# Kernel tuning notes

Hardware: AMD Instinct MI355X
Metric: run time of the kernel (lower is better)

Reference implementation:

```python
import jax, jax.numpy as jnp
import numpy as np

N, E, IN, OUT, R, B = 20000, 640000, 128, 128, 64, 16


def setup_inputs() -> dict:
    key = jax.random.key(0)
    ks = jax.random.split(key, 9)
    xav_w = float(np.sqrt(2.0 / (IN + OUT)))  # xavier-uniform-ish scale
    xav_c = float(np.sqrt(2.0 / (R + B)))
    return {
        "x": jax.random.normal(ks[0], (N, IN), jnp.float32),
        "weight": jax.random.normal(ks[1], (B, IN, OUT), jnp.float32) * xav_w,
        "w_comp": jax.random.normal(ks[2], (R, B), jnp.float32) * xav_c,
        "h_bias": jnp.zeros((OUT,), jnp.float32),
        "loop_weight": jax.random.normal(ks[3], (IN, OUT), jnp.float32) * xav_w,
        "norm": jax.random.uniform(ks[4], (E, 1), jnp.float32),
        "src": jax.random.randint(ks[5], (E,), 0, N, jnp.int32),
        "dst": jax.random.randint(ks[6], (E,), 0, N, jnp.int32),
        "etypes": jax.random.randint(ks[7], (E,), 0, R, jnp.int32),
    }


def reference(x, weight, w_comp, h_bias, loop_weight, norm, src, dst, etypes):
    # Basis composition: per-relation weights W_rel[r] = sum_b w_comp[r,b] * weight[b]
    W_rel = jnp.einsum("rb,bio->rio", w_comp, weight)          # [R, IN, OUT]
    # Project every node through every relation weight (N*R << per-edge bmm
    # of E gathered [IN,OUT] matrices; same math as bmm_maybe_select).
    h_all = jnp.einsum("ni,rio->nro", x, W_rel)                 # [N, R, OUT]
    # Per-edge message: msg_e = x[src_e] @ W_rel[etype_e], scaled by norm
    msg = h_all[src, etypes] * norm                              # [E, OUT]
    # fn.sum aggregation to destination nodes
    agg = jax.ops.segment_sum(msg, dst, num_segments=x.shape[0])  # [N, OUT]
    out = agg + h_bias + x @ loop_weight                          # bias + self-loop
    return jax.nn.relu(out)                                       # activation; dropout p=0
```

## Files before the change

### kernel.cpp

```cpp
#include <hip/hip_runtime.h>

#define N_NODES 20000
#define E_EDGES 640000
#define R_REL   64
#define B_BASES 16
#define NSEG    128
#define SEGLEN  (E_EDGES / NSEG)
#define RH      10000
#define NBPR    16
#define QG      ((2 * NSEG) / 16)

typedef __attribute__((ext_vector_type(4))) float f32x4;
typedef __attribute__((ext_vector_type(8))) _Float16 half8;

__device__ inline float h2f(unsigned short v) {
    _Float16 h; __builtin_memcpy(&h, &v, 2); return (float)h;
}
__device__ inline unsigned short f2h(float f) {
    _Float16 h = (_Float16)f; unsigned short v; __builtin_memcpy(&v, &h, 2); return v;
}

__device__ inline void gld_lds16(const void* g, void* l) {
    __builtin_amdgcn_global_load_lds(
        (const __attribute__((address_space(1))) void*)g,
        (__attribute__((address_space(3))) void*)l, 16, 0, 0);
}


__global__ void k_wrelh(const float* weight, const float* w_comp, unsigned short* wt_h)
{
    __shared__ float tile[32][33];
    __shared__ float wcS[B_BASES];
    int r  = blockIdx.x >> 4;
    int ti = (blockIdx.x >> 2) & 3;
    int tj = blockIdx.x & 3;
    int tx = threadIdx.x & 31, ty = threadIdx.x >> 5;
    if (threadIdx.x < B_BASES) wcS[threadIdx.x] = w_comp[r * B_BASES + threadIdx.x];
    __syncthreads();
    float acc[4] = {0.f, 0.f, 0.f, 0.f};
    const float* wp = weight + (ti * 32) * 128 + tj * 32;
    for (int b = 0; b < B_BASES; b++) {
        float c = wcS[b];
        #pragma unroll
        for (int s = 0; s < 4; s++)
            acc[s] += c * wp[b * 16384 + (ty + s * 8) * 128 + tx];
    }
    #pragma unroll
    for (int s = 0; s < 4; s++) tile[ty + s * 8][tx] = acc[s];
    __syncthreads();
    unsigned short* dstp = wt_h + r * 16384 + (tj * 32) * 128 + ti * 32;
    #pragma unroll
    for (int s = 0; s < 4; s++)
        dstp[(ty + s * 8) * 128 + tx] = f2h(tile[tx][ty + s * 8]);
}

__global__ void k_lwh(const float* lw, unsigned short* lwT)
{
    __shared__ float tile[32][33];
    int ti = blockIdx.x >> 2, tj = blockIdx.x & 3;
    int tx = threadIdx.x & 31, ty = threadIdx.x >> 5;
    const float* srcp = lw + (ti * 32) * 128 + tj * 32;
    #pragma unroll
    for (int s = 0; s < 4; s++)
        tile[ty + s * 8][tx] = srcp[(ty + s * 8) * 128 + tx];
    __syncthreads();
    unsigned short* d = lwT + (tj * 32) * 128 + ti * 32;
    #pragma unroll
    for (int s = 0; s < 4; s++)
        d[(ty + s * 8) * 128 + tx] = f2h(tile[tx][ty + s * 8]);
}

__global__ void k_xhalf(const float* x, unsigned short* xh)
{
    int i4 = blockIdx.x * 256 + threadIdx.x;
    float4 v = ((const float4*)x)[i4];
    ushort4 o;
    o.x = f2h(v.x); o.y = f2h(v.y); o.z = f2h(v.z); o.w = f2h(v.w);
    ((ushort4*)xh)[i4] = o;
}

__global__ void k_histp(const int* etypes, const int* dst, int* hp, int* he)
{
    __shared__ int lh[RH];
    __shared__ int heL[R_REL];
    int t = threadIdx.x, q = blockIdx.x;
    int s = q >> 1, h = q & 1;
    for (int i = t; i < RH; i += 256) lh[i] = 0;
    if (t < R_REL) heL[t] = 0;
    __syncthreads();
    int e0 = s * SEGLEN;
    for (int k = t; k < SEGLEN; k += 256) {
        int e = e0 + k;
        int d = dst[e];
        unsigned ld = (unsigned)(d - h * RH);
        if (ld < RH) {
            atomicAdd(&lh[ld], 1);
            atomicAdd(&heL[etypes[e]], 1);
        }
    }
    __syncthreads();
    for (int i = t; i < RH; i += 256) hp[s * N_NODES + h * RH + i] = lh[i];
    if (t < R_REL) he[q * 64 + t] = heL[t];
}

__global__ void k_sumc(const int* hp, int* counts2)
{
    int n = blockIdx.x * 256 + threadIdx.x;
    if (n >= N_NODES) return;
    int s = 0;
    for (int q = 0; q < NSEG; q += 8) {
        int v[8];
        #pragma unroll
        for (int k = 0; k < 8; k++) v[k] = hp[(q + k) * N_NODES + n];
        #pragma unroll
        for (int k = 0; k < 8; k++) s += v[k];
    }
    counts2[n] = s;
}

__global__ void k_scan_all2(const int* he, const int* counts2,
                            int* offsets, int* off2, int* be)
{
    __shared__ int part[1024];
    __shared__ int psum[16][R_REL];
    __shared__ int offL[R_REL];
    int tid = threadIdx.x;
    int t = tid & 63;
    int g = tid >> 6;
    int vals[QG];
    int ps = 0;
    #pragma unroll
    for (int k = 0; k < QG; k++) {
        vals[k] = he[(g * QG + k) * 64 + t];
        ps += vals[k];
    }
    psum[g][t] = ps;
    __syncthreads();
    if (tid < 64) {
        int c = 0;
        #pragma unroll
        for (int gg = 0; gg < 16; gg++) c += psum[gg][t];
        int s1 = c;
        for (int d = 1; d < 64; d <<= 1) {
            int a1 = __shfl_up(s1, d);
            if (t >= d) s1 += a1;
        }
        offsets[t] = s1 - c;
        offL[t] = s1 - c;
        if (t == 63) offsets[64] = s1;
    }
    __syncthreads();
    {
        int run = offL[t];
        for (int gg = 0; gg < g; gg++) run += psum[gg][t];
        #pragma unroll
        for (int k = 0; k < QG; k++) {
            be[(g * QG + k) * 64 + t] = run;
            run += vals[k];
        }
    }
    int lo_i = tid * 20, hi_i = lo_i + 20;
    if (hi_i > N_NODES) hi_i = N_NODES;
    if (lo_i > N_NODES) lo_i = N_NODES;
    int s = 0;
    for (int i = lo_i; i < hi_i; i++) s += counts2[i];
    part[tid] = s;
    __syncthreads();
    for (int d = 1; d < 1024; d <<= 1) {
        int v = (tid >= d) ? part[tid - d] : 0;
        __syncthreads();
        part[tid] += v;
        __syncthreads();
    }
    int run = part[tid] - s;
    for (int i = lo_i; i < hi_i; i++) {
        off2[i] = run;
        run += counts2[i];
    }
    if (tid == 1023) off2[N_NODES] = run;
}

__global__ void k_segbase(const int* off2, int* hp)
{
    int n = blockIdx.x * 256 + threadIdx.x;
    if (n >= N_NODES) return;
    int run = off2[n];
    for (int q = 0; q < NSEG; q += 8) {
        int v[8];
        #pragma unroll
        for (int k = 0; k < 8; k++) v[k] = hp[(q + k) * N_NODES + n];
        #pragma unroll
        for (int k = 0; k < 8; k++) { hp[(q + k) * N_NODES + n] = run; run += v[k]; }
    }
}

__global__ void k_scatter3(const int* etypes, const int* dst, const int* src, const float* norm,
                           const int* hp, const int* be,
                           int* perm_src, float* pnorm, int* pos2)
{
    __shared__ int lbase[RH];
    __shared__ int ebase[R_REL];
    int t = threadIdx.x, q = blockIdx.x;
    int s = q >> 1, h = q & 1;
    for (int i = t; i < RH; i += 256) lbase[i] = hp[s * N_NODES + h * RH + i];
    if (t < R_REL) ebase[t] = be[q * 64 + t];
    __syncthreads();
    int e0 = s * SEGLEN;
    for (int k = t; k < SEGLEN; k += 256) {
        int e = e0 + k;
        int d = dst[e];
        unsigned ld = (unsigned)(d - h * RH);
        if (ld < RH) {
            int slot = atomicAdd(&lbase[ld], 1);
            int p = atomicAdd(&ebase[etypes[e]], 1);
            perm_src[p] = src[e];
            pnorm[p] = norm[e];
            pos2[p] = slot;
        }
    }
}

__global__ __launch_bounds__(256) void k_edge_mfma(
    const unsigned short* __restrict__ xh, const unsigned short* __restrict__ wt_h,
    const int* __restrict__ perm_src, const float* __restrict__ pnorm,
    const int* __restrict__ pos2, const int* __restrict__ offsets,
    unsigned short* __restrict__ msg)
{
    __shared__ __align__(16) char smemW[32768];
    int t = threadIdx.x, b = blockIdx.x;
    int r = b >> 4;
    int j = b & (NBPR - 1);
    int p0 = offsets[r], p1 = offsets[r + 1];
    int nch = (p1 - p0 + 63) >> 6;

    {
        const size_t rbase = (size_t)r * 16384;
        #pragma unroll
        for (int it = 0; it < 8; it++) {
            int s = it * 256 + t;
            int o = s >> 4, ch = s & 15;
            int jx = ch ^ (o & 15);
            gld_lds16(wt_h + rbase + o * 128 + jx * 8, smemW + s * 16);
        }
    }

    int l = t & 63, w = t >> 6;
    int lg = l >> 4, lr = l & 15;
    int wr = w >> 1, wc = w & 1;
    int rowA0 = wr * 32 + lr, rowA1 = rowA0 + 16;
    const half8* smW = (const half8*)smemW;

    int i = j;
    int sA0 = 0, sA1 = 0;
    if (i < nch) {
        int e0 = p0 + i * 64;
        int cnt = p1 - e0; if (cnt > 64) cnt = 64;
        sA0 = (rowA0 < cnt) ? perm_src[e0 + rowA0] : 0;
        sA1 = (rowA1 < cnt) ? perm_src[e0 + rowA1] : 0;
    }

    __syncthreads();

    while (i < nch) {
        int e0 = p0 + i * 64;
        int cnt = p1 - e0; if (cnt > 64) cnt = 64;

        int slotC[2][4]; float nrmC[2][4];
        #pragma unroll
        for (int a = 0; a < 2; a++)
            #pragma unroll
            for (int jj = 0; jj < 4; jj++) {
                int row = wr * 32 + a * 16 + lg * 4 + jj;
                bool vld = row < cnt;
                slotC[a][jj] = vld ? pos2[e0 + row] : -1;
                nrmC[a][jj]  = vld ? pnorm[e0 + row] : 0.0f;
            }

        const half8* xr0 = (const half8*)(xh + (size_t)sA0 * 128);
        const half8* xr1 = (const half8*)(xh + (size_t)sA1 * 128);
        half8 av0[4], av1[4];
        #pragma unroll
        for (int kk = 0; kk < 4; kk++) {
            av0[kk] = xr0[kk * 4 + lg];
            av1[kk] = xr1[kk * 4 + lg];
        }

        int inext = i + NBPR;
        if (inext < nch) {
            int e0n = p0 + inext * 64;
            int cntn = p1 - e0n; if (cntn > 64) cntn = 64;
            sA0 = (rowA0 < cntn) ? perm_src[e0n + rowA0] : 0;
            sA1 = (rowA1 < cntn) ? perm_src[e0n + rowA1] : 0;
        }

        f32x4 acc[2][4];
        #pragma unroll
        for (int a = 0; a < 2; a++)
            #pragma unroll
            for (int n = 0; n < 4; n++)
                acc[a][n] = {0.0f, 0.0f, 0.0f, 0.0f};

        #pragma unroll
        for (int kk = 0; kk < 4; kk++) {
            #pragma unroll
            for (int n = 0; n < 4; n++) {
                int o = wc * 64 + n * 16 + lr;
                half8 bv = smW[o * 16 + ((kk * 4 + lg) ^ (o & 15))];
                acc[0][n] = __builtin_amdgcn_mfma_f32_16x16x32_f16(av0[kk], bv, acc[0][n], 0, 0, 0);
                acc[1][n] = __builtin_amdgcn_mfma_f32_16x16x32_f16(av1[kk], bv, acc[1][n], 0, 0, 0);
            }
        }

        #pragma unroll
        for (int a = 0; a < 2; a++)
            #pragma unroll
            for (int jj = 0; jj < 4; jj++) {
                int slot = slotC[a][jj];
                if (slot >= 0) {
                    float nm = nrmC[a][jj];
                    unsigned int q0 = (unsigned int)f2h(acc[a][0][jj] * nm)
                                    | ((unsigned int)f2h(acc[a][1][jj] * nm) << 16);
                    unsigned int q1 = (unsigned int)f2h(acc[a][2][jj] * nm)
                                    | ((unsigned int)f2h(acc[a][3][jj] * nm) << 16);
                    uint2 ov; ov.x = q0; ov.y = q1;
                    *(uint2*)(msg + (size_t)slot * 128 + wc * 64 + lr * 4) = ov;
                }
            }
        i = inext;
    }
}

__global__ __launch_bounds__(256) void k_selfmfma(
    const unsigned short* __restrict__ xh, const unsigned short* __restrict__ lwT,
    float* __restrict__ out)
{
    __shared__ __align__(16) char smemW[32768];
    int t = threadIdx.x, b = blockIdx.x;
    int n0 = b * 64;

    #pragma unroll
    for (int it = 0; it < 8; it++) {
        int s = it * 256 + t;
        int o = s >> 4, ch = s & 15;
        int jx = ch ^ (o & 15);
        gld_lds16(lwT + o * 128 + jx * 8, smemW + s * 16);
    }

    int l = t & 63, w = t >> 6;
    int lg = l >> 4, lr = l & 15;
    int wr = w >> 1, wc = w & 1;
    int rowA0 = wr * 32 + lr, rowA1 = rowA0 + 16;
    int nA0 = n0 + rowA0; if (nA0 >= N_NODES) nA0 = N_NODES - 1;
    int nA1 = n0 + rowA1; if (nA1 >= N_NODES) nA1 = N_NODES - 1;
    const half8* xr0 = (const half8*)(xh + (size_t)nA0 * 128);
    const half8* xr1 = (const half8*)(xh + (size_t)nA1 * 128);
    half8 av0[4], av1[4];
    #pragma unroll
    for (int kk = 0; kk < 4; kk++) {
        av0[kk] = xr0[kk * 4 + lg];
        av1[kk] = xr1[kk * 4 + lg];
    }

    f32x4 acc[2][4];
    #pragma unroll
    for (int a = 0; a < 2; a++)
        #pragma unroll
        for (int n = 0; n < 4; n++)
            acc[a][n] = {0.0f, 0.0f, 0.0f, 0.0f};

    __syncthreads();

    const half8* smW = (const half8*)smemW;
    #pragma unroll
    for (int kk = 0; kk < 4; kk++) {
        #pragma unroll
        for (int n = 0; n < 4; n++) {
            int o = wc * 64 + n * 16 + lr;
            half8 bv = smW[o * 16 + ((kk * 4 + lg) ^ (o & 15))];
            acc[0][n] = __builtin_amdgcn_mfma_f32_16x16x32_f16(av0[kk], bv, acc[0][n], 0, 0, 0);
            acc[1][n] = __builtin_amdgcn_mfma_f32_16x16x32_f16(av1[kk], bv, acc[1][n], 0, 0, 0);
        }
    }

    #pragma unroll
    for (int a = 0; a < 2; a++)
        #pragma unroll
        for (int jj = 0; jj < 4; jj++) {
            int row = wr * 32 + a * 16 + lg * 4 + jj;
            int n = n0 + row;
            if (n < N_NODES) {
                float4 v;
                v.x = acc[a][0][jj]; v.y = acc[a][1][jj];
                v.z = acc[a][2][jj]; v.w = acc[a][3][jj];
                *(float4*)(out + (size_t)n * 128 + wc * 64 + lr * 4) = v;
            }
        }
}

__global__ void k_msgsum(const unsigned short* msg, const int* off2,
                         const float* bias, float* out)
{
    __shared__ float4 red[256];
    __shared__ float fin[128];
    int n = blockIdx.x, t = threadIdx.x;
    int m0 = off2[n], m1 = off2[n + 1];
    int rp = t >> 5, c = t & 31;
    float4 a; a.x = 0.f; a.y = 0.f; a.z = 0.f; a.w = 0.f;
    for (int j = m0 + rp; j < m1; j += 8) {
        uint2 v = *(const uint2*)(msg + (size_t)j * 128 + c * 4);
        a.x += h2f((unsigned short)(v.x & 0xffff));
        a.y += h2f((unsigned short)(v.x >> 16));
        a.z += h2f((unsigned short)(v.y & 0xffff));
        a.w += h2f((unsigned short)(v.y >> 16));
    }
    red[t] = a;
    __syncthreads();
    if (t < 128) {
        float4 b = red[t + 128];
        red[t].x += b.x; red[t].y += b.y; red[t].z += b.z; red[t].w += b.w;
    }
    __syncthreads();
    if (t < 64) {
        float4 b = red[t + 64];
        red[t].x += b.x; red[t].y += b.y; red[t].z += b.z; red[t].w += b.w;
    }
    __syncthreads();
    if (t < 32) {
        float4 v = red[t], b = red[t + 32];
        v.x += b.x; v.y += b.y; v.z += b.z; v.w += b.w;
        float4 o = *(const float4*)(out + (size_t)n * 128 + t * 4);
        v.x += o.x; v.y += o.y; v.z += o.z; v.w += o.w;
        int base = (t >> 4) * 64 + (t & 15);
        fin[base]      = v.x;
        fin[base + 16] = v.y;
        fin[base + 32] = v.z;
        fin[base + 48] = v.w;
    }
    __syncthreads();
    if (t < 32) {
        float4 f = ((const float4*)fin)[t];
        float4 bb = *(const float4*)(bias + t * 4);
        f.x += bb.x; f.y += bb.y; f.z += bb.z; f.w += bb.w;
        if (f.x < 0.f) f.x = 0.f;
        if (f.y < 0.f) f.y = 0.f;
        if (f.z < 0.f) f.z = 0.f;
        if (f.w < 0.f) f.w = 0.f;
        *(float4*)(out + (size_t)n * 128 + t * 4) = f;
    }
}


__global__ void k_wrel(const float* weight, const float* w_comp, float* W_rel)
{
    int idx = blockIdx.x * 256 + threadIdx.x;
    int r  = idx >> 14;
    int io = idx & 16383;
    float acc = 0.0f;
    for (int b = 0; b < B_BASES; b++)
        acc += w_comp[r * B_BASES + b] * weight[b * 16384 + io];
    W_rel[idx] = acc;
}

__global__ void k_zero(float* agg, int* counts, int* counts2)
{
    int idx = blockIdx.x * 256 + threadIdx.x;
    if (idx < N_NODES * 128) agg[idx] = 0.0f;
    if (idx < R_REL) counts[idx] = 0;
    if (idx < N_NODES) counts2[idx] = 0;
}

__global__ void k_hist(const int* etypes, int* counts)
{
    __shared__ int h[R_REL];
    int t = threadIdx.x;
    if (t < R_REL) h[t] = 0;
    __syncthreads();
    int e = blockIdx.x * 256 + t;
    atomicAdd(&h[etypes[e]], 1);
    __syncthreads();
    if (t < R_REL && h[t] != 0) atomicAdd(&counts[t], h[t]);
}

__global__ void k_scan(const int* counts, int* offsets, int* cursor, int* co)
{
    if (threadIdx.x == 0) {
        int run = 0, c = 0;
        for (int r = 0; r < R_REL; r++) {
            offsets[r] = run; cursor[r] = run; co[r] = c;
            run += counts[r];
            c   += (counts[r] + 63) >> 6;
        }
        offsets[R_REL] = run; co[R_REL] = c;
    }
}

__global__ void k_scatter(const int* etypes, int* cursor, int* perm)
{
    __shared__ int h[R_REL];
    __shared__ int base[R_REL];
    int t = threadIdx.x;
    if (t < R_REL) h[t] = 0;
    __syncthreads();
    int e = blockIdx.x * 256 + t;
    int et = etypes[e];
    int rank = atomicAdd(&h[et], 1);
    __syncthreads();
    if (t < R_REL && h[t] != 0) base[t] = atomicAdd(&cursor[t], h[t]);
    __syncthreads();
    perm[base[et] + rank] = e;
}

__global__ void k_edge_atomic(const float* x, const float* W_rel, const float* norm,
                              const int* src, const int* dst, const int* perm,
                              const int* offsets, const int* co, float* agg)
{
    __shared__ float4 WfS[2048];
    __shared__ float4 xsS[1024];
    __shared__ int coS[R_REL + 1];
    __shared__ int srcS[64], dstS[64];
    __shared__ float normS[64];
    int t = threadIdx.x, bid = blockIdx.x;
    if (t <= R_REL) coS[t] = co[t];
    __syncthreads();
    if (bid >= coS[R_REL]) return;
    int r = 0;
    while (bid >= coS[r + 1]) r++;
    int e0 = offsets[r] + (bid - coS[r]) * 64;
    int cnt = offsets[r + 1] - e0;
    if (cnt > 64) cnt = 64;
    if (t < 64) {
        if (t < cnt) {
            int eid = perm[e0 + t];
            srcS[t] = src[eid]; dstS[t] = dst[eid]; normS[t] = norm[eid];
        } else { srcS[t] = 0; dstS[t] = 0; normS[t] = 0.0f; }
    }
    const float* xsf = (const float*)xsS;
    int q  = t & 31;
    int eb = t >> 5;
    float4 acc[8];
    for (int k = 0; k < 8; k++) { acc[k].x = 0.f; acc[k].y = 0.f; acc[k].z = 0.f; acc[k].w = 0.f; }
    for (int h = 0; h < 2; h++) {
        __syncthreads();
        const float4* Wsrc = (const float4*)(W_rel + r * 16384 + h * 8192);
        for (int p = 0; p < 8; p++) WfS[p * 256 + t] = Wsrc[p * 256 + t];
        for (int p = 0; p < 4; p++) {
            int idx = p * 256 + t;
            int e = idx >> 4, c = idx & 15;
            xsS[idx] = ((const float4*)(x + srcS[e] * 128 + h * 64))[c];
        }
        __syncthreads();
        for (int i = 0; i < 64; i++) {
            float4 wv = WfS[i * 32 + q];
            for (int k = 0; k < 8; k++) {
                float xv = xsf[(eb + 8 * k) * 64 + i];
                acc[k].x += xv * wv.x;
                acc[k].y += xv * wv.y;
                acc[k].z += xv * wv.z;
                acc[k].w += xv * wv.w;
            }
        }
    }
    for (int k = 0; k < 8; k++) {
        int e = eb + 8 * k;
        if (e < cnt) {
            float nrm = normS[e];
            float* row = agg + dstS[e] * 128 + q * 4;
            atomicAdd(row + 0, acc[k].x * nrm);
            atomicAdd(row + 1, acc[k].y * nrm);
            atomicAdd(row + 2, acc[k].z * nrm);
            atomicAdd(row + 3, acc[k].w * nrm);
        }
    }
}

__global__ void k_out(const float* x, const float* loop_w, const float* agg,
                      const float* bias, float* out)
{
    __shared__ float xrow[128];
    int n = blockIdx.x;
    int o = threadIdx.x;
    xrow[o] = x[n * 128 + o];
    __syncthreads();
    float acc = 0.0f;
    for (int i = 0; i < 128; i++)
        acc += xrow[i] * loop_w[i * 128 + o];
    float val = acc + agg[n * 128 + o] + bias[o];
    if (val < 0.0f) val = 0.0f;
    out[n * 128 + o] = val;
}

extern "C" void kernel_launch(void* const* d_in, const int* in_sizes, int n_in,
                              void* d_out, int out_size, void* d_ws, size_t ws_size,
                              hipStream_t stream)
{
    const float* x      = (const float*)d_in[0];
    const float* weight = (const float*)d_in[1];
    const float* w_comp = (const float*)d_in[2];
    const float* h_bias = (const float*)d_in[3];
    const float* loop_w = (const float*)d_in[4];
    const float* norm   = (const float*)d_in[5];
    const int* src    = (const int*)d_in[6];
    const int* dst    = (const int*)d_in[7];
    const int* etypes = (const int*)d_in[8];
    float* out = (float*)d_out;

    char* ws = (char*)d_ws;
    size_t off = 0;
    float* W_rel = (float*)(ws + off); off += (size_t)R_REL * 16384 * 4;
    float* agg   = (float*)(ws + off); off += (size_t)N_NODES * 128 * 4;
    int* perm    = (int*)(ws + off);   off += (size_t)E_EDGES * 4;
    int* counts  = (int*)(ws + off);   off += 64 * 4;
    int* offsets = (int*)(ws + off);   off += 68 * 4;
    int* cursor  = (int*)(ws + off);   off += 64 * 4;
    int* co      = (int*)(ws + off);   off += 68 * 4;
    int* counts2 = (int*)(ws + off);   off += (size_t)N_NODES * 4;
    int* off2    = (int*)(ws + off);   off += (size_t)(N_NODES + 4) * 4;
    int* cursor2 = (int*)(ws + off);   off += (size_t)N_NODES * 4;
    int* pos2    = (int*)(ws + off);   off += (size_t)E_EDGES * 4;
    unsigned short* msg = (unsigned short*)(ws + off);
    size_t need_big = off + (size_t)E_EDGES * 128 * 2;
    int big = (ws_size >= need_big) ? 1 : 0;

    if (big) {
        unsigned short* wt_h = (unsigned short*)W_rel;
        char* wspare = (char*)W_rel + (size_t)2 * 1024 * 1024;
        unsigned short* lwT = (unsigned short*)wspare;
        unsigned short* xh = (unsigned short*)agg;
        float* pnorm = (float*)((char*)agg + (size_t)N_NODES * 128 * 2);
        int* perm_src = perm;
        int* hp = (int*)msg;
        int* he = (int*)((char*)msg + (size_t)NSEG * N_NODES * 4);
        int* be = (int*)((char*)he + (size_t)2 * NSEG * 64 * 4);

        k_wrelh<<<R_REL * 16, 256, 0, stream>>>(weight, w_comp, wt_h);
        k_lwh<<<16, 256, 0, stream>>>(loop_w, lwT);
        k_xhalf<<<(N_NODES * 128 / 4) / 256, 256, 0, stream>>>(x, xh);
        k_histp<<<2 * NSEG, 256, 0, stream>>>(etypes, dst, hp, he);
        k_sumc<<<(N_NODES + 255) / 256, 256, 0, stream>>>(hp, counts2);
        k_scan_all2<<<1, 1024, 0, stream>>>(he, counts2, offsets, off2, be);
        k_segbase<<<(N_NODES + 255) / 256, 256, 0, stream>>>(off2, hp);
        k_scatter3<<<2 * NSEG, 256, 0, stream>>>(etypes, dst, src, norm,
                                                 hp, be, perm_src, pnorm, pos2);
        k_edge_mfma<<<R_REL * NBPR, 256, 0, stream>>>(
            xh, wt_h, perm_src, pnorm, pos2, offsets, msg);
        k_selfmfma<<<(N_NODES + 63) / 64, 256, 0, stream>>>(xh, lwT, out);
        k_msgsum<<<N_NODES, 256, 0, stream>>>(msg, off2, h_bias, out);
    } else {
        k_wrel<<<(R_REL * 16384) / 256, 256, 0, stream>>>(weight, w_comp, W_rel);
        k_zero<<<(N_NODES * 128) / 256, 256, 0, stream>>>(agg, counts, counts2);
        k_hist<<<E_EDGES / 256, 256, 0, stream>>>(etypes, counts);
        k_scan<<<1, 64, 0, stream>>>(counts, offsets, cursor, co);
        k_scatter<<<E_EDGES / 256, 256, 0, stream>>>(etypes, cursor, perm);
        k_edge_atomic<<<E_EDGES / 64 + R_REL, 256, 0, stream>>>(
            x, W_rel, norm, src, dst, perm, offsets, co, agg);
        k_out<<<N_NODES, 128, 0, stream>>>(x, loop_w, agg, h_bias, out);
    }
}
```

Baseline: 274.8 us.

## Retile edge MFMA per-wave, prefetch gathered rows, double blocks per relation, fuse weight prep

The edge and self-loop MFMA kernels now give each wave 16 rows across all 128 output columns instead of a 2x2 wave split. Each lane writes 16-byte message stores, and the msgsum epilogue's column permutation is changed to match the new output layout. The edge kernel now prefetches the next chunk's gathered x rows into registers one iteration ahead, and blocks per relation go from 16 to 32 for more parallelism and latency hiding. The loop-weight transpose kernel is folded into the relation-weight kernel to save a launch. The trade-off is higher register pressure from the 8 accumulators plus the prefetch buffers, and each block reloading the 32KB weight tile into LDS twice as often.

Measured after the change: 266.4 us. 3.0% less time.

```diff
diff --git a/kernel.cpp b/kernel.cpp
--- a/kernel.cpp
+++ b/kernel.cpp
@@ -7,7 +7,7 @@
 #define NSEG    128
 #define SEGLEN  (E_EDGES / NSEG)
 #define RH      10000
-#define NBPR    16
+#define NBPR    32
 #define QG      ((2 * NSEG) / 16)
 
 typedef __attribute__((ext_vector_type(4))) float f32x4;
@@ -27,14 +27,30 @@
 }
 
 
-__global__ void k_wrelh(const float* weight, const float* w_comp, unsigned short* wt_h)
+__global__ void k_wrelh(const float* weight, const float* w_comp, unsigned short* wt_h,
+                        const float* lw, unsigned short* lwT)
 {
     __shared__ float tile[32][33];
     __shared__ float wcS[B_BASES];
-    int r  = blockIdx.x >> 4;
-    int ti = (blockIdx.x >> 2) & 3;
-    int tj = blockIdx.x & 3;
+    int bid = blockIdx.x;
     int tx = threadIdx.x & 31, ty = threadIdx.x >> 5;
+    if (bid >= R_REL * 16) {
+        int q = bid - R_REL * 16;
+        int ti = q >> 2, tj = q & 3;
+        const float* srcp = lw + (ti * 32) * 128 + tj * 32;
+        #pragma unroll
+        for (int s = 0; s < 4; s++)
+            tile[ty + s * 8][tx] = srcp[(ty + s * 8) * 128 + tx];
+        __syncthreads();
+        unsigned short* d = lwT + (tj * 32) * 128 + ti * 32;
+        #pragma unroll
+        for (int s = 0; s < 4; s++)
+            d[(ty + s * 8) * 128 + tx] = f2h(tile[tx][ty + s * 8]);
+        return;
+    }
+    int r  = bid >> 4;
+    int ti = (bid >> 2) & 3;
+    int tj = bid & 3;
     if (threadIdx.x < B_BASES) wcS[threadIdx.x] = w_comp[r * B_BASES + threadIdx.x];
     __syncthreads();
     float acc[4] = {0.f, 0.f, 0.f, 0.f};
@@ -52,22 +68,6 @@
     #pragma unroll
     for (int s = 0; s < 4; s++)
         dstp[(ty + s * 8) * 128 + tx] = f2h(tile[tx][ty + s * 8]);
-}
-
-__global__ void k_lwh(const float* lw, unsigned short* lwT)
-{
-    __shared__ float tile[32][33];
-    int ti = blockIdx.x >> 2, tj = blockIdx.x & 3;
-    int tx = threadIdx.x & 31, ty = threadIdx.x >> 5;
-    const float* srcp = lw + (ti * 32) * 128 + tj * 32;
-    #pragma unroll
-    for (int s = 0; s < 4; s++)
-        tile[ty + s * 8][tx] = srcp[(ty + s * 8) * 128 + tx];
-    __syncthreads();
-    unsigned short* d = lwT + (tj * 32) * 128 + ti * 32;
-    #pragma unroll
-    for (int s = 0; s < 4; s++)
-        d[(ty + s * 8) * 128 + tx] = f2h(tile[tx][ty + s * 8]);
 }
 
 __global__ void k_xhalf(const float* x, unsigned short* xh)
@@ -228,7 +228,7 @@
 {
     __shared__ __align__(16) char smemW[32768];
     int t = threadIdx.x, b = blockIdx.x;
-    int r = b >> 4;
+    int r = b >> 5;
     int j = b & (NBPR - 1);
     int p0 = offsets[r], p1 = offsets[r + 1];
     int nch = (p1 - p0 + 63) >> 6;
@@ -246,87 +246,89 @@
 
     int l = t & 63, w = t >> 6;
     int lg = l >> 4, lr = l & 15;
-    int wr = w >> 1, wc = w & 1;
-    int rowA0 = wr * 32 + lr, rowA1 = rowA0 + 16;
+    int rowA = w * 16 + lr;
     const half8* smW = (const half8*)smemW;
 
     int i = j;
-    int sA0 = 0, sA1 = 0;
+    int sN = 0;
     if (i < nch) {
         int e0 = p0 + i * 64;
         int cnt = p1 - e0; if (cnt > 64) cnt = 64;
-        sA0 = (rowA0 < cnt) ? perm_src[e0 + rowA0] : 0;
-        sA1 = (rowA1 < cnt) ? perm_src[e0 + rowA1] : 0;
-    }
-
-    __syncthreads();
+        sN = (rowA < cnt) ? perm_src[e0 + rowA] : 0;
+    }
+
+    __syncthreads();
+
+    half8 avC[4];
+    {
+        const half8* xr = (const half8*)(xh + (size_t)sN * 128);
+        #pragma unroll
+        for (int kk = 0; kk < 4; kk++) avC[kk] = xr[kk * 4 + lg];
+    }
+    int i2 = i + NBPR;
+    if (i2 < nch) {
+        int e0 = p0 + i2 * 64;
+        int cnt = p1 - e0; if (cnt > 64) cnt = 64;
+        sN = (rowA < cnt) ? perm_src[e0 + rowA] : 0;
+    }
 
     while (i < nch) {
         int e0 = p0 + i * 64;
         int cnt = p1 - e0; if (cnt > 64) cnt = 64;
 
-        int slotC[2][4]; float nrmC[2][4];
-        #pragma unroll
-        for (int a = 0; a < 2; a++)
+        int slotC[4]; float nrmC[4];
+        #pragma unroll
+        for (int jj = 0; jj < 4; jj++) {
+            int row = w * 16 + lg * 4 + jj;
+            bool vld = row < cnt;
+            slotC[jj] = vld ? pos2[e0 + row] : -1;
+            nrmC[jj]  = vld ? pnorm[e0 + row] : 0.0f;
+        }
+
+        half8 avN[4];
+        {
+            const half8* xr = (const half8*)(xh + (size_t)sN * 128);
             #pragma unroll
-            for (int jj = 0; jj < 4; jj++) {
-                int row = wr * 32 + a * 16 + lg * 4 + jj;
-                bool vld = row < cnt;
-                slotC[a][jj] = vld ? pos2[e0 + row] : -1;
-                nrmC[a][jj]  = vld ? pnorm[e0 + row] : 0.0f;
-            }
-
-        const half8* xr0 = (const half8*)(xh + (size_t)sA0 * 128);
-        const half8* xr1 = (const half8*)(xh + (size_t)sA1 * 128);
-        half8 av0[4], av1[4];
-        #pragma unroll
-        for (int kk = 0; kk < 4; kk++) {
-            av0[kk] = xr0[kk * 4 + lg];
-            av1[kk] = xr1[kk * 4 + lg];
-        }
-
-        int inext = i + NBPR;
-        if (inext < nch) {
-            int e0n = p0 + inext * 64;
+            for (int kk = 0; kk < 4; kk++) avN[kk] = xr[kk * 4 + lg];
+        }
+        int i3 = i2 + NBPR;
+        if (i3 < nch) {
+            int e0n = p0 + i3 * 64;
             int cntn = p1 - e0n; if (cntn > 64) cntn = 64;
-            sA0 = (rowA0 < cntn) ? perm_src[e0n + rowA0] : 0;
-            sA1 = (rowA1 < cntn) ? perm_src[e0n + rowA1] : 0;
-        }
-
-        f32x4 acc[2][4];
-        #pragma unroll
-        for (int a = 0; a < 2; a++)
-            #pragma unroll
-            for (int n = 0; n < 4; n++)
-                acc[a][n] = {0.0f, 0.0f, 0.0f, 0.0f};
+            sN = (rowA < cntn) ? perm_src[e0n + rowA] : 0;
+        }
+
+        f32x4 acc[8];
+        #pragma unroll
+        for (int n = 0; n < 8; n++) acc[n] = {0.0f, 0.0f, 0.0f, 0.0f};
 
         #pragma unroll
         for (int kk = 0; kk < 4; kk++) {
             #pragma unroll
-            for (int n = 0; n < 4; n++) {
-                int o = wc * 64 + n * 16 + lr;
+            for (int n = 0; n < 8; n++) {
+                int o = n * 16 + lr;
                 half8 bv = smW[o * 16 + ((kk * 4 + lg) ^ (o & 15))];
-                acc[0][n] = __builtin_amdgcn_mfma_f32_16x16x32_f16(av0[kk], bv, acc[0][n], 0, 0, 0);
-                acc[1][n] = __builtin_amdgcn_mfma_f32_16x16x32_f16(av1[kk], bv, acc[1][n], 0, 0, 0);
+                acc[n] = __builtin_amdgcn_mfma_f32_16x16x32_f16(avC[kk], bv, acc[n], 0, 0, 0);
             }
         }
 
         #pragma unroll
-        for (int a = 0; a < 2; a++)
-            #pragma unroll
-            for (int jj = 0; jj < 4; jj++) {
-                int slot = slotC[a][jj];
-                if (slot >= 0) {
-                    float nm = nrmC[a][jj];
-                    unsigned int q0 = (unsigned int)f2h(acc[a][0][jj] * nm)
-                                    | ((unsigned int)f2h(acc[a][1][jj] * nm) << 16);
-                    unsigned int q1 = (unsigned int)f2h(acc[a][2][jj] * nm)
-                                    | ((unsigned int)f2h(acc[a][3][jj] * nm) << 16);
-                    uint2 ov; ov.x = q0; ov.y = q1;
-                    *(uint2*)(msg + (size_t)slot * 128 + wc * 64 + lr * 4) = ov;
-                }
+        for (int jj = 0; jj < 4; jj++) {
+            int slot = slotC[jj];
+            if (slot >= 0) {
+                float nm = nrmC[jj];
+                uint4 ov;
+                ov.x = (unsigned int)f2h(acc[0][jj] * nm) | ((unsigned int)f2h(acc[1][jj] * nm) << 16);
+                ov.y = (unsigned int)f2h(acc[2][jj] * nm) | ((unsigned int)f2h(acc[3][jj] * nm) << 16);
+                ov.z = (unsigned int)f2h(acc[4][jj] * nm) | ((unsigned int)f2h(acc[5][jj] * nm) << 16);
+                ov.w = (unsigned int)f2h(acc[6][jj] * nm) | ((unsigned int)f2h(acc[7][jj] * nm) << 16);
+                *(uint4*)(msg + (size_t)slot * 128 + lr * 8) = ov;
             }
-        i = inext;
+        }
+
+        #pragma unroll
+        for (int kk = 0; kk < 4; kk++) avC[kk] = avN[kk];
+        i = i2; i2 = i3;
     }
 }
 
@@ -348,53 +350,42 @@
 
     int l = t & 63, w = t >> 6;
     int lg = l >> 4, lr = l & 15;
-    int wr = w >> 1, wc = w & 1;
-    int rowA0 = wr * 32 + lr, rowA1 = rowA0 + 16;
-    int nA0 = n0 + rowA0; if (nA0 >= N_NODES) nA0 = N_NODES - 1;
-    int nA1 = n0 + rowA1; if (nA1 >= N_NODES) nA1 = N_NODES - 1;
-    const half8* xr0 = (const half8*)(xh + (size_t)nA0 * 128);
-    const half8* xr1 = (const half8*)(xh + (size_t)nA1 * 128);
-    half8 av0[4], av1[4];
+    int rowA = w * 16 + lr;
+    int nA = n0 + rowA; if (nA >= N_NODES) nA = N_NODES - 1;
+    const half8* xr = (const half8*)(xh + (size_t)nA * 128);
+    half8 avC[4];
+    #pragma unroll
+    for (int kk = 0; kk < 4; kk++) avC[kk] = xr[kk * 4 + lg];
+
+    f32x4 acc[8];
+    #pragma unroll
+    for (int n = 0; n < 8; n++) acc[n] = {0.0f, 0.0f, 0.0f, 0.0f};
+
+    __syncthreads();
+
+    const half8* smW = (const half8*)smemW;
     #pragma unroll
     for (int kk = 0; kk < 4; kk++) {
-        av0[kk] = xr0[kk * 4 + lg];
-        av1[kk] = xr1[kk * 4 + lg];
-    }
-
-    f32x4 acc[2][4];
-    #pragma unroll
-    for (int a = 0; a < 2; a++)
-        #pragma unroll
-        for (int n = 0; n < 4; n++)
-            acc[a][n] = {0.0f, 0.0f, 0.0f, 0.0f};
-
-    __syncthreads();
-
-    const half8* smW = (const half8*)smemW;
-    #pragma unroll
-    for (int kk = 0; kk < 4; kk++) {
-        #pragma unroll
-        for (int n = 0; n < 4; n++) {
-            int o = wc * 64 + n * 16 + lr;
+        #pragma unroll
+        for (int n = 0; n < 8; n++) {
+            int o = n * 16 + lr;
             half8 bv = smW[o * 16 + ((kk * 4 + lg) ^ (o & 15))];
-            acc[0][n] = __builtin_amdgcn_mfma_f32_16x16x32_f16(av0[kk], bv, acc[0][n], 0, 0, 0);
-            acc[1][n] = __builtin_amdgcn_mfma_f32_16x16x32_f16(av1[kk], bv, acc[1][n], 0, 0, 0);
-        }
-    }
-
-    #pragma unroll
-    for (int a = 0; a < 2; a++)
-        #pragma unroll
-        for (int jj = 0; jj < 4; jj++) {
-            int row = wr * 32 + a * 16 + lg * 4 + jj;
-            int n = n0 + row;
-            if (n < N_NODES) {
-                float4 v;
-                v.x = acc[a][0][jj]; v.y = acc[a][1][jj];
-                v.z = acc[a][2][jj]; v.w = acc[a][3][jj];
-                *(float4*)(out + (size_t)n * 128 + wc * 64 + lr * 4) = v;
-            }
-        }
+            acc[n] = __builtin_amdgcn_mfma_f32_16x16x32_f16(avC[kk], bv, acc[n], 0, 0, 0);
+        }
+    }
+
+    #pragma unroll
+    for (int jj = 0; jj < 4; jj++) {
+        int row = w * 16 + lg * 4 + jj;
+        int n = n0 + row;
+        if (n < N_NODES) {
+            float4 v0, v1;
+            v0.x = acc[0][jj]; v0.y = acc[1][jj]; v0.z = acc[2][jj]; v0.w = acc[3][jj];
+            v1.x = acc[4][jj]; v1.y = acc[5][jj]; v1.z = acc[6][jj]; v1.w = acc[7][jj];
+            *(float4*)(out + (size_t)n * 128 + lr * 8) = v0;
+            *(float4*)(out + (size_t)n * 128 + lr * 8 + 4) = v1;
+        }
+    }
 }
 
 __global__ void k_msgsum(const unsigned short* msg, const int* off2,
@@ -430,7 +421,7 @@
         v.x += b.x; v.y += b.y; v.z += b.z; v.w += b.w;
         float4 o = *(const float4*)(out + (size_t)n * 128 + t * 4);
         v.x += o.x; v.y += o.y; v.z += o.z; v.w += o.w;
-        int base = (t >> 4) * 64 + (t & 15);
+        int base = (t & 1) * 64 + (t >> 1);
         fin[base]      = v.x;
         fin[base + 16] = v.y;
         fin[base + 32] = v.z;
@@ -632,8 +623,7 @@
         int* he = (int*)((char*)msg + (size_t)NSEG * N_NODES * 4);
         int* be = (int*)((char*)he + (size_t)2 * NSEG * 64 * 4);
 
-        k_wrelh<<<R_REL * 16, 256, 0, stream>>>(weight, w_comp, wt_h);
-        k_lwh<<<16, 256, 0, stream>>>(loop_w, lwT);
+        k_wrelh<<<R_REL * 16 + 16, 256, 0, stream>>>(weight, w_comp, wt_h, loop_w, lwT);
         k_xhalf<<<(N_NODES * 128 / 4) / 256, 256, 0, stream>>>(x, xh);
         k_histp<<<2 * NSEG, 256, 0, stream>>>(etypes, dst, hp, he);
         k_sumc<<<(N_NODES + 255) / 256, 256, 0, stream>>>(hp, counts2);
```
